# Performance work log

Hardware: AMD Instinct MI355X
Metric: run time of the kernel (lower is better)

The kernel has to match this reference:

```python
import jax, jax.numpy as jnp
import numpy as np
from math import factorial, sqrt

# (mul, l) lists after e3nn normalization/mul-splitting (muls already aligned)
RS1 = [(256, 0), (256, 1), (256, 2)]
RS2 = [(256, 1), (256, 1), (256, 2)]


def _su2_cg(j1, m1, j2, m2, j3, m3):
    # Racah formula for SU(2) Clebsch-Gordan <j1 m1 j2 m2 | j3 m3> (e3nn convention)
    if m3 != m1 + m2:
        return 0.0
    vmin = max(-j1 + j2 + m3, -j1 + m1, 0)
    vmax = min(j2 + j3 + m1, j3 - j1 + j2, j3 + m3)
    f = factorial
    C = sqrt((2 * j3 + 1)
             * f(j3 + j1 - j2) * f(j3 - j1 + j2) * f(j1 + j2 - j3) * f(j3 + m3) * f(j3 - m3)
             / (f(j1 + j2 + j3 + 1) * f(j1 - m1) * f(j1 + m1) * f(j2 - m2) * f(j2 + m2)))
    S = 0.0
    for v in range(vmin, vmax + 1):
        S += (-1.0) ** (v + j2 + m2) * (f(j2 + j3 + m1 - v) * f(j1 - m1 + v)
             / (f(v) * f(j3 - j1 + j2 - v) * f(j3 + m3 - v) * f(v + j1 - j2 - m3)))
    return C * S


def _su2_cg_tensor(j1, j2, j3):
    mat = np.zeros((2 * j1 + 1, 2 * j2 + 1, 2 * j3 + 1))
    for m1 in range(-j1, j1 + 1):
        for m2 in range(-j2, j2 + 1):
            m3 = m1 + m2
            if abs(m3) <= j3:
                mat[j1 + m1, j2 + m2, j3 + m3] = _su2_cg(j1, m1, j2, m2, j3, m3)
    return mat / sqrt(2 * j3 + 1)  # Wigner-3j normalization


def _q(l):
    # change of basis real -> complex spherical harmonics (e3nn convention)
    q = np.zeros((2 * l + 1, 2 * l + 1), dtype=np.complex128)
    for m in range(-l, 0):
        q[l + m, l + abs(m)] = 1.0 / sqrt(2)
        q[l + m, l - abs(m)] = -1j / sqrt(2)
    q[l, l] = 1.0
    for m in range(1, l + 1):
        q[l + m, l + abs(m)] = (-1) ** m / sqrt(2)
        q[l + m, l - abs(m)] = 1j * (-1) ** m / sqrt(2)
    return (-1j) ** l * q


def _wigner3j(l1, l2, l3):
    # real-basis Wigner 3j tensor, shape (2l1+1, 2l2+1, 2l3+1)
    C = _su2_cg_tensor(l1, l2, l3)
    Q1, Q2, Q3 = _q(l1), _q(l2), _q(l3)
    C = np.einsum('ij,kl,nm,ikn->jlm', Q1, Q2, np.conj(Q3), C)
    assert np.abs(C.imag).max() < 1e-6
    return C.real


# precomputed CG blocks C[(l, l1, l2)] of shape (2l+1, 2l1+1, 2l2+1), scaled by sqrt(2l+1)
CG = {}
for (_mul1, _l1), (_mul2, _l2) in zip(RS1, RS2):
    if _l1 != 0 and _l2 != 0:
        for _l in range(abs(_l1 - _l2), _l1 + _l2 + 1):
            CG[(_l, _l1, _l2)] = jnp.asarray(_wigner3j(_l, _l1, _l2) * sqrt(2 * _l + 1), dtype=jnp.float32)


def _forward(features_1, features_2):
    size = features_1.shape[:-1]
    f1 = features_1.reshape(-1, features_1.shape[-1])
    f2 = features_2.reshape(-1, features_2.shape[-1])
    B = f1.shape[0]
    out, i1, i2 = [], 0, 0
    for (mul, l1), (_, l2) in zip(RS1, RS2):
        d1, d2 = 2 * l1 + 1, 2 * l2 + 1
        x1 = f1[:, i1:i1 + mul * d1].reshape(B, mul, d1)
        i1 += mul * d1
        x2 = f2[:, i2:i2 + mul * d2].reshape(B, mul, d2)
        i2 += mul * d2
        if l1 == 0 or l2 == 0:
            # CG with a scalar is (a multiple of) identity -> elementwise product
            out.append((x1 * x2).reshape(B, -1))
        else:
            for l in range(abs(l1 - l2), l1 + l2 + 1):
                C = CG[(l, l1, l2)]  # (2l+1, d1, d2)
                out.append(jnp.einsum('ijk,bmj,bmk->bmi', C, x1, x2).reshape(B, -1))
    return jnp.concatenate(out, axis=1).reshape(*size, -1)


def setup_inputs() -> dict:
    key = jax.random.key(0)
    k1, k2 = jax.random.split(key)
    n1 = sum(m * (2 * l + 1) for m, l in RS1)  # 2304
    n2 = sum(m * (2 * l + 1) for m, l in RS2)  # 2816
    B = 8192
    return {
        'features_1': jax.random.normal(k1, (B, n1), dtype=jnp.float32),
        'features_2': jax.random.normal(k2, (B, n2), dtype=jnp.float32),
    }


def reference(features_1, features_2):
    return _forward(features_1, features_2)
```

## Files before the change

kernel.cpp:

```cpp
#include <hip/hip_runtime.h>

namespace cg {

constexpr double fact(int n) {
  double r = 1.0;
  for (int i = 2; i <= n; ++i) r *= (double)i;
  return r;
}

constexpr double csqrt(double x) {
  if (x <= 0.0) return 0.0;
  double g = x < 1.0 ? 1.0 : x;
  for (int i = 0; i < 80; ++i) g = 0.5 * (g + x / g);
  return g;
}

struct cplx { double re, im; };
constexpr cplx cmul(cplx a, cplx b) {
  return cplx{a.re * b.re - a.im * b.im, a.re * b.im + a.im * b.re};
}

constexpr double su2_cg(int j1, int m1, int j2, int m2, int j3, int m3) {
  if (m3 != m1 + m2) return 0.0;
  int vmin = -j1 + j2 + m3;
  if (-j1 + m1 > vmin) vmin = -j1 + m1;
  if (0 > vmin) vmin = 0;
  int vmax = j2 + j3 + m1;
  if (j3 - j1 + j2 < vmax) vmax = j3 - j1 + j2;
  if (j3 + m3 < vmax) vmax = j3 + m3;
  const double C = csqrt((2.0 * j3 + 1.0)
      * fact(j3 + j1 - j2) * fact(j3 - j1 + j2) * fact(j1 + j2 - j3)
      * fact(j3 + m3) * fact(j3 - m3)
      / (fact(j1 + j2 + j3 + 1) * fact(j1 - m1) * fact(j1 + m1)
         * fact(j2 - m2) * fact(j2 + m2)));
  double S = 0.0;
  for (int v = vmin; v <= vmax; ++v) {
    const double sgn = ((v + j2 + m2) & 1) ? -1.0 : 1.0;
    S += sgn * (fact(j2 + j3 + m1 - v) * fact(j1 - m1 + v)
         / (fact(v) * fact(j3 - j1 + j2 - v) * fact(j3 + m3 - v)
            * fact(v + j1 - j2 - m3)));
  }
  return C * S;
}

template <int L> struct QMat { cplx q[2 * L + 1][2 * L + 1]; };

template <int L>
constexpr QMat<L> make_q() {
  QMat<L> Q{};
  const double s = 1.0 / csqrt(2.0);
  for (int m = -L; m < 0; ++m) {
    Q.q[L + m][L - m] = cplx{s, 0.0};
    Q.q[L + m][L + m] = cplx{0.0, -s};
  }
  Q.q[L][L] = cplx{1.0, 0.0};
  for (int m = 1; m <= L; ++m) {
    const double sg = (m & 1) ? -1.0 : 1.0;
    Q.q[L + m][L + m] = cplx{sg * s, 0.0};
    Q.q[L + m][L - m] = cplx{0.0, sg * s};
  }
  cplx p{1.0, 0.0};
  for (int t = 0; t < L; ++t) p = cmul(p, cplx{0.0, -1.0});
  for (int r = 0; r < 2 * L + 1; ++r)
    for (int c = 0; c < 2 * L + 1; ++c)
      Q.q[r][c] = cmul(p, Q.q[r][c]);
  return Q;
}

template <int L, int L1, int L2>
struct W3 { float t[2 * L + 1][2 * L1 + 1][2 * L2 + 1]; };

template <int L, int L1, int L2>
constexpr W3<L, L1, L2> wigner() {
  const QMat<L>  Q1 = make_q<L>();
  const QMat<L1> Q2 = make_q<L1>();
  const QMat<L2> Q3 = make_q<L2>();
  double C[2 * L + 1][2 * L1 + 1][2 * L2 + 1] = {};
  for (int m1 = -L; m1 <= L; ++m1)
    for (int m2 = -L1; m2 <= L1; ++m2) {
      const int m3 = m1 + m2;
      if (m3 >= -L2 && m3 <= L2)
        C[L + m1][L1 + m2][L2 + m3] = su2_cg(L, m1, L1, m2, L2, m3);
    }
  const double scale = csqrt(2.0 * L + 1.0) / csqrt(2.0 * L2 + 1.0);
  W3<L, L1, L2> R{};
  for (int j = 0; j < 2 * L + 1; ++j)
    for (int l = 0; l < 2 * L1 + 1; ++l)
      for (int m = 0; m < 2 * L2 + 1; ++m) {
        cplx acc{0.0, 0.0};
        for (int i = 0; i < 2 * L + 1; ++i) {
          const cplx q1 = Q1.q[i][j];
          if (q1.re == 0.0 && q1.im == 0.0) continue;
          for (int k = 0; k < 2 * L1 + 1; ++k) {
            const cplx q2 = Q2.q[k][l];
            if (q2.re == 0.0 && q2.im == 0.0) continue;
            const cplx q12 = cmul(q1, q2);
            for (int n = 0; n < 2 * L2 + 1; ++n) {
              const double c = C[i][k][n];
              if (c == 0.0) continue;
              const cplx q3c{Q3.q[n][m].re, -Q3.q[n][m].im};
              const cplx term = cmul(q12, q3c);
              acc.re += term.re * c;
              acc.im += term.im * c;
            }
          }
        }
        R.t[j][l][m] = (float)(acc.re * scale);
      }
  return R;
}

constexpr W3<0, 1, 1> W011 = wigner<0, 1, 1>();
constexpr W3<1, 1, 1> W111 = wigner<1, 1, 1>();
constexpr W3<2, 1, 1> W211 = wigner<2, 1, 1>();
constexpr W3<0, 2, 2> W022 = wigner<0, 2, 2>();
constexpr W3<1, 2, 2> W122 = wigner<1, 2, 2>();
constexpr W3<2, 2, 2> W222 = wigner<2, 2, 2>();
constexpr W3<3, 2, 2> W322 = wigner<3, 2, 2>();
constexpr W3<4, 2, 2> W422 = wigner<4, 2, 2>();

}


template <int L, int L1, int L2>
__device__ __forceinline__ void contract(const cg::W3<L, L1, L2>& W,
                                         const float (&p)[2 * L1 + 1][2 * L2 + 1],
                                         float* __restrict__ o) {
#pragma unroll
  for (int i = 0; i < 2 * L + 1; ++i) {
    float acc = 0.0f;
#pragma unroll
    for (int j = 0; j < 2 * L1 + 1; ++j)
#pragma unroll
      for (int k = 0; k < 2 * L2 + 1; ++k) {
        const float c = W.t[i][j][k];
        if (c != 0.0f) acc = __builtin_fmaf(c, p[j][k], acc);
      }
    o[i] = acc;
  }
}

__global__ __launch_bounds__(64) void tp_kernel(
    const float* __restrict__ f1, const float* __restrict__ f2,
    float* __restrict__ out, int B) {
  __shared__ __align__(16) float Wr[2368];
  const int bid = blockIdx.x;
  const int b = bid >> 2;
  if (b >= B) return;
  const int w = bid & 3;
  const int l = threadIdx.x;

  {
    const float4* s1 = reinterpret_cast<const float4*>(f1 + (size_t)b * 2304);
    const float4* s2 = reinterpret_cast<const float4*>(f2 + (size_t)b * 2816);
    float4* L4 = reinterpret_cast<float4*>(Wr);
    if (l < 16) L4[l] = s1[16 * w + l];
    if (l < 48) L4[16 + l] = s1[64 + 48 * w + l];
    L4[64 + l] = s1[256 + 80 * w + l];
    if (l < 16) L4[128 + l] = s1[256 + 80 * w + 64 + l];
    if (l < 48) L4[144 + l] = s2[48 * w + l];
    if (l < 48) L4[192 + l] = s2[192 + 48 * w + l];
    L4[240 + l] = s2[384 + 80 * w + l];
    if (l < 16) L4[304 + l] = s2[384 + 80 * w + 64 + l];
  }
  __syncthreads();

  const float s0 = Wr[l];
  float ca[3], a1[3], cb[3], a2[5], cc[5];
#pragma unroll
  for (int k = 0; k < 3; ++k) ca[k] = Wr[576 + l * 3 + k];
#pragma unroll
  for (int j = 0; j < 3; ++j) a1[j] = Wr[64 + l * 3 + j];
#pragma unroll
  for (int k = 0; k < 3; ++k) cb[k] = Wr[768 + l * 3 + k];
#pragma unroll
  for (int j = 0; j < 5; ++j) a2[j] = Wr[256 + l * 5 + j];
#pragma unroll
  for (int k = 0; k < 5; ++k) cc[k] = Wr[960 + l * 5 + k];

  float r0[3];
#pragma unroll
  for (int k = 0; k < 3; ++k) r0[k] = s0 * ca[k];

  float o0, o1[3], o2[5];
  {
    float p[3][3];
#pragma unroll
    for (int j = 0; j < 3; ++j)
#pragma unroll
      for (int k = 0; k < 3; ++k) p[j][k] = a1[j] * cb[k];
    contract<0, 1, 1>(cg::W011, p, &o0);
    contract<1, 1, 1>(cg::W111, p, o1);
    contract<2, 1, 1>(cg::W211, p, o2);
  }
  float q0, q1[3], q2[5], q3[7], q4[9];
  {
    float p[5][5];
#pragma unroll
    for (int j = 0; j < 5; ++j)
#pragma unroll
      for (int k = 0; k < 5; ++k) p[j][k] = a2[j] * cc[k];
    contract<0, 2, 2>(cg::W022, p, &q0);
    contract<1, 2, 2>(cg::W122, p, q1);
    contract<2, 2, 2>(cg::W222, p, q2);
    contract<3, 2, 2>(cg::W322, p, q3);
    contract<4, 2, 2>(cg::W422, p, q4);
  }
  __syncthreads();

#pragma unroll
  for (int k = 0; k < 3; ++k) Wr[l * 3 + k] = r0[k];
  Wr[192 + l] = o0;
#pragma unroll
  for (int i = 0; i < 3; ++i) Wr[256 + l * 3 + i] = o1[i];
#pragma unroll
  for (int i = 0; i < 5; ++i) Wr[448 + l * 5 + i] = o2[i];
  Wr[768 + l] = q0;
#pragma unroll
  for (int i = 0; i < 3; ++i) Wr[832 + l * 3 + i] = q1[i];
#pragma unroll
  for (int i = 0; i < 5; ++i) Wr[1024 + l * 5 + i] = q2[i];
#pragma unroll
  for (int i = 0; i < 7; ++i) Wr[1344 + l * 7 + i] = q3[i];
#pragma unroll
  for (int i = 0; i < 9; ++i) Wr[1792 + l * 9 + i] = q4[i];
  __syncthreads();

  {
    const float4* OF = reinterpret_cast<const float4*>(Wr);
    float4* D = reinterpret_cast<float4*>(out + (size_t)b * 9472);
    if (l < 48) D[48 * w + l] = OF[l];
    if (l < 16) D[192 + 16 * w + l] = OF[48 + l];
    if (l < 48) D[256 + 48 * w + l] = OF[64 + l];
    D[448 + 80 * w + l] = OF[112 + l];
    if (l < 16) D[448 + 80 * w + 64 + l] = OF[176 + l];
    if (l < 16) D[768 + 16 * w + l] = OF[192 + l];
    if (l < 48) D[832 + 48 * w + l] = OF[208 + l];
    D[1024 + 80 * w + l] = OF[256 + l];
    if (l < 16) D[1024 + 80 * w + 64 + l] = OF[320 + l];
    D[1344 + 112 * w + l] = OF[336 + l];
    if (l < 48) D[1344 + 112 * w + 64 + l] = OF[400 + l];
    D[1792 + 144 * w + l] = OF[448 + l];
    D[1792 + 144 * w + 64 + l] = OF[512 + l];
    if (l < 16) D[1792 + 144 * w + 128 + l] = OF[576 + l];
  }
}

extern "C" void kernel_launch(void* const* d_in, const int* in_sizes, int n_in,
                              void* d_out, int out_size, void* d_ws, size_t ws_size,
                              hipStream_t stream) {
  const float* f1 = (const float*)d_in[0];
  const float* f2 = (const float*)d_in[1];
  float* out = (float*)d_out;
  const int B = in_sizes[0] / 2304;
  tp_kernel<<<B * 4, 64, 0, stream>>>(f1, f2, out, B);
}
```

Baseline: 96.90 us.

## Process four rows per block with direct global loads and prefetch of next row

Each 256-thread block now handles four batch rows; every wave takes one quarter of the channels, and each thread loads its 20 input values straight from global memory (strided scalar loads) instead of staging them through LDS with float4 copies. The next row's inputs are prefetched into registers while the current row's outputs are written, and the output transpose through per-wave LDS relies on wave-local ordering with compiler memory fences instead of __syncthreads. This cuts block count and barriers and overlaps loads with stores, but uses uncoalesced strided input reads, more registers, and a larger 37 KB LDS footprint that reduces occupancy.

```diff
diff --git a/kernel.cpp b/kernel.cpp
--- a/kernel.cpp
+++ b/kernel.cpp
@@ -140,109 +140,118 @@
   }
 }
 
-__global__ __launch_bounds__(64) void tp_kernel(
+__device__ __forceinline__ void load_inputs(const float* __restrict__ f1,
+                                            const float* __restrict__ f2,
+                                            size_t r, int m, float (&in)[20]) {
+  const float* F1 = f1 + r * 2304;
+  const float* F2 = f2 + r * 2816;
+  in[0] = F1[m];
+#pragma unroll
+  for (int j = 0; j < 3; ++j) in[1 + j] = F1[256 + m * 3 + j];
+#pragma unroll
+  for (int j = 0; j < 5; ++j) in[4 + j] = F1[1024 + m * 5 + j];
+#pragma unroll
+  for (int k = 0; k < 3; ++k) in[9 + k] = F2[m * 3 + k];
+#pragma unroll
+  for (int k = 0; k < 3; ++k) in[12 + k] = F2[768 + m * 3 + k];
+#pragma unroll
+  for (int k = 0; k < 5; ++k) in[15 + k] = F2[1536 + m * 5 + k];
+}
+
+__global__ __launch_bounds__(256) void tp_kernel(
     const float* __restrict__ f1, const float* __restrict__ f2,
     float* __restrict__ out, int B) {
-  __shared__ __align__(16) float Wr[2368];
-  const int bid = blockIdx.x;
-  const int b = bid >> 2;
-  if (b >= B) return;
-  const int w = bid & 3;
-  const int l = threadIdx.x;
-
-  {
-    const float4* s1 = reinterpret_cast<const float4*>(f1 + (size_t)b * 2304);
-    const float4* s2 = reinterpret_cast<const float4*>(f2 + (size_t)b * 2816);
-    float4* L4 = reinterpret_cast<float4*>(Wr);
-    if (l < 16) L4[l] = s1[16 * w + l];
-    if (l < 48) L4[16 + l] = s1[64 + 48 * w + l];
-    L4[64 + l] = s1[256 + 80 * w + l];
-    if (l < 16) L4[128 + l] = s1[256 + 80 * w + 64 + l];
-    if (l < 48) L4[144 + l] = s2[48 * w + l];
-    if (l < 48) L4[192 + l] = s2[192 + 48 * w + l];
-    L4[240 + l] = s2[384 + 80 * w + l];
-    if (l < 16) L4[304 + l] = s2[384 + 80 * w + 64 + l];
-  }
-  __syncthreads();
-
-  const float s0 = Wr[l];
-  float ca[3], a1[3], cb[3], a2[5], cc[5];
-#pragma unroll
-  for (int k = 0; k < 3; ++k) ca[k] = Wr[576 + l * 3 + k];
-#pragma unroll
-  for (int j = 0; j < 3; ++j) a1[j] = Wr[64 + l * 3 + j];
-#pragma unroll
-  for (int k = 0; k < 3; ++k) cb[k] = Wr[768 + l * 3 + k];
-#pragma unroll
-  for (int j = 0; j < 5; ++j) a2[j] = Wr[256 + l * 5 + j];
-#pragma unroll
-  for (int k = 0; k < 5; ++k) cc[k] = Wr[960 + l * 5 + k];
-
-  float r0[3];
-#pragma unroll
-  for (int k = 0; k < 3; ++k) r0[k] = s0 * ca[k];
-
-  float o0, o1[3], o2[5];
-  {
-    float p[3][3];
-#pragma unroll
-    for (int j = 0; j < 3; ++j)
-#pragma unroll
-      for (int k = 0; k < 3; ++k) p[j][k] = a1[j] * cb[k];
-    contract<0, 1, 1>(cg::W011, p, &o0);
-    contract<1, 1, 1>(cg::W111, p, o1);
-    contract<2, 1, 1>(cg::W211, p, o2);
-  }
-  float q0, q1[3], q2[5], q3[7], q4[9];
-  {
-    float p[5][5];
-#pragma unroll
-    for (int j = 0; j < 5; ++j)
-#pragma unroll
-      for (int k = 0; k < 5; ++k) p[j][k] = a2[j] * cc[k];
-    contract<0, 2, 2>(cg::W022, p, &q0);
-    contract<1, 2, 2>(cg::W122, p, q1);
-    contract<2, 2, 2>(cg::W222, p, q2);
-    contract<3, 2, 2>(cg::W322, p, q3);
-    contract<4, 2, 2>(cg::W422, p, q4);
-  }
-  __syncthreads();
-
-#pragma unroll
-  for (int k = 0; k < 3; ++k) Wr[l * 3 + k] = r0[k];
-  Wr[192 + l] = o0;
-#pragma unroll
-  for (int i = 0; i < 3; ++i) Wr[256 + l * 3 + i] = o1[i];
-#pragma unroll
-  for (int i = 0; i < 5; ++i) Wr[448 + l * 5 + i] = o2[i];
-  Wr[768 + l] = q0;
-#pragma unroll
-  for (int i = 0; i < 3; ++i) Wr[832 + l * 3 + i] = q1[i];
-#pragma unroll
-  for (int i = 0; i < 5; ++i) Wr[1024 + l * 5 + i] = q2[i];
-#pragma unroll
-  for (int i = 0; i < 7; ++i) Wr[1344 + l * 7 + i] = q3[i];
-#pragma unroll
-  for (int i = 0; i < 9; ++i) Wr[1792 + l * 9 + i] = q4[i];
-  __syncthreads();
-
-  {
-    const float4* OF = reinterpret_cast<const float4*>(Wr);
-    float4* D = reinterpret_cast<float4*>(out + (size_t)b * 9472);
-    if (l < 48) D[48 * w + l] = OF[l];
-    if (l < 16) D[192 + 16 * w + l] = OF[48 + l];
-    if (l < 48) D[256 + 48 * w + l] = OF[64 + l];
-    D[448 + 80 * w + l] = OF[112 + l];
-    if (l < 16) D[448 + 80 * w + 64 + l] = OF[176 + l];
-    if (l < 16) D[768 + 16 * w + l] = OF[192 + l];
-    if (l < 48) D[832 + 48 * w + l] = OF[208 + l];
-    D[1024 + 80 * w + l] = OF[256 + l];
-    if (l < 16) D[1024 + 80 * w + 64 + l] = OF[320 + l];
-    D[1344 + 112 * w + l] = OF[336 + l];
-    if (l < 48) D[1344 + 112 * w + 64 + l] = OF[400 + l];
-    D[1792 + 144 * w + l] = OF[448 + l];
-    D[1792 + 144 * w + 64 + l] = OF[512 + l];
-    if (l < 16) D[1792 + 144 * w + 128 + l] = OF[576 + l];
+  __shared__ __align__(16) float lds[9472];
+  const int w = threadIdx.x >> 6;
+  const int l = threadIdx.x & 63;
+  const int m = 64 * w + l;
+  float* Wr = lds + w * 2368;
+
+  const int row0 = blockIdx.x * 4;
+  if (row0 >= B) return;
+
+  float in[20], in2[20];
+  load_inputs(f1, f2, (size_t)row0, m, in);
+
+#pragma unroll
+  for (int i = 0; i < 4; ++i) {
+    const int r = row0 + i;
+
+    float r0[3];
+#pragma unroll
+    for (int k = 0; k < 3; ++k) r0[k] = in[0] * in[9 + k];
+
+    float o0, o1[3], o2[5];
+    {
+      float p[3][3];
+#pragma unroll
+      for (int j = 0; j < 3; ++j)
+#pragma unroll
+        for (int k = 0; k < 3; ++k) p[j][k] = in[1 + j] * in[12 + k];
+      contract<0, 1, 1>(cg::W011, p, &o0);
+      contract<1, 1, 1>(cg::W111, p, o1);
+      contract<2, 1, 1>(cg::W211, p, o2);
+    }
+    float q0, q1[3], q2[5], q3[7], q4[9];
+    {
+      float p[5][5];
+#pragma unroll
+      for (int j = 0; j < 5; ++j)
+#pragma unroll
+        for (int k = 0; k < 5; ++k) p[j][k] = in[4 + j] * in[15 + k];
+      contract<0, 2, 2>(cg::W022, p, &q0);
+      contract<1, 2, 2>(cg::W122, p, q1);
+      contract<2, 2, 2>(cg::W222, p, q2);
+      contract<3, 2, 2>(cg::W322, p, q3);
+      contract<4, 2, 2>(cg::W422, p, q4);
+    }
+
+    if (i < 3 && r + 1 < B) load_inputs(f1, f2, (size_t)(r + 1), m, in2);
+
+#pragma unroll
+    for (int k = 0; k < 3; ++k) Wr[l * 3 + k] = r0[k];
+    Wr[192 + l] = o0;
+#pragma unroll
+    for (int k = 0; k < 3; ++k) Wr[256 + l * 3 + k] = o1[k];
+#pragma unroll
+    for (int k = 0; k < 5; ++k) Wr[448 + l * 5 + k] = o2[k];
+    Wr[768 + l] = q0;
+#pragma unroll
+    for (int k = 0; k < 3; ++k) Wr[832 + l * 3 + k] = q1[k];
+#pragma unroll
+    for (int k = 0; k < 5; ++k) Wr[1024 + l * 5 + k] = q2[k];
+#pragma unroll
+    for (int k = 0; k < 7; ++k) Wr[1344 + l * 7 + k] = q3[k];
+#pragma unroll
+    for (int k = 0; k < 9; ++k) Wr[1792 + l * 9 + k] = q4[k];
+
+    asm volatile("" ::: "memory");
+
+    {
+      const float4* OF = reinterpret_cast<const float4*>(Wr);
+      float4* D = reinterpret_cast<float4*>(out + (size_t)r * 9472);
+      if (l < 48) D[48 * w + l] = OF[l];
+      if (l < 16) D[192 + 16 * w + l] = OF[48 + l];
+      if (l < 48) D[256 + 48 * w + l] = OF[64 + l];
+      D[448 + 80 * w + l] = OF[112 + l];
+      if (l < 16) D[448 + 80 * w + 64 + l] = OF[176 + l];
+      if (l < 16) D[768 + 16 * w + l] = OF[192 + l];
+      if (l < 48) D[832 + 48 * w + l] = OF[208 + l];
+      D[1024 + 80 * w + l] = OF[256 + l];
+      if (l < 16) D[1024 + 80 * w + 64 + l] = OF[320 + l];
+      D[1344 + 112 * w + l] = OF[336 + l];
+      if (l < 48) D[1344 + 112 * w + 64 + l] = OF[400 + l];
+      D[1792 + 144 * w + l] = OF[448 + l];
+      D[1792 + 144 * w + 64 + l] = OF[512 + l];
+      if (l < 16) D[1792 + 144 * w + 128 + l] = OF[576 + l];
+    }
+
+    asm volatile("" ::: "memory");
+
+    if (i < 3) {
+#pragma unroll
+      for (int k = 0; k < 20; ++k) in[k] = in2[k];
+    }
   }
 }
 
@@ -253,5 +262,5 @@
   const float* f2 = (const float*)d_in[1];
   float* out = (float*)d_out;
   const int B = in_sizes[0] / 2304;
-  tp_kernel<<<B * 4, 64, 0, stream>>>(f1, f2, out, B);
-}
+  tp_kernel<<<(B + 3) / 4, 256, 0, stream>>>(f1, f2, out, B);
+}
```

New measurement: 101.3 us. 4.5% more time.
